# Kernel tuning notes

Measured on AMD Instinct MI355X. Metric: run time of the kernel, lower is better.

The kernel has to match this reference:

```python
import jax, jax.numpy as jnp
import numpy as np
from jax import lax

EPSILON = 1e-12


def _sobel_kernels(n1=1, n2=2, n3=2):
    Sx = np.asarray([[[-n1, 0, n1], [-n2, 0, n2], [-n1, 0, n1]],
                     [[-n2, 0, n2], [-n3 * n2, 0, n3 * n2], [-n2, 0, n2]],
                     [[-n1, 0, n1], [-n2, 0, n2], [-n1, 0, n1]]])
    Sy = np.asarray([[[-n1, -n2, -n1], [0, 0, 0], [n1, n2, n1]],
                     [[-n2, -n3 * n2, -n2], [0, 0, 0], [n2, n3 * n2, n2]],
                     [[-n1, -n2, -n1], [0, 0, 0], [n1, n2, n1]]])
    Sz = np.asarray([[[-n1, -n2, -n1], [-n2, -n3 * n2, -n2], [-n1, -n2, -n1]],
                     [[0, 0, 0], [0, 0, 0], [0, 0, 0]],
                     [[n1, n2, n1], [n2, n3 * n2, n2], [n1, n2, n1]]])
    Sd11 = np.asarray([[[0, n1, n2], [-n1, 0, n1], [-n2, -n1, 0]],
                       [[0, n2, n2 * n3], [-n2, 0, n2], [-n2 * n3, -n2, 0]],
                       [[0, n1, n2], [-n1, 0, n1], [-n2, -n1, 0]]])
    Sd12 = np.asarray([[[-n2, -n1, 0], [-n1, 0, n1], [0, n1, n2]],
                       [[-n2 * n3, -n2, 0], [-n2, 0, n2], [0, n2, n2 * n3]],
                       [[-n2, -n1, 0], [-n1, 0, n1], [0, n1, n2]]])
    Sd21 = Sd11.T
    Sd22 = Sd12.T
    Sd31 = np.asarray([-S.T for S in Sd11.T])
    Sd32 = np.asarray([S.T for S in Sd12.T])
    ks = np.stack([Sx, Sy, Sz, Sd11, Sd12, Sd21, Sd22, Sd31, Sd32]).astype(np.float32)
    return jnp.asarray(ks[:, None])  # [9, 1, 3, 3, 3] (OIDHW)


_KERNELS = _sobel_kernels(1, 2, 2)


def _edge_magnitude(img):
    # img: [B, C, H, W, D]. Per-channel convs are summed over C in the original;
    # by linearity of conv, sum channels first, then run all 9 stencils at once.
    C = img.shape[1]
    x = jnp.sum(img, axis=1, keepdims=True)  # [B, 1, H, W, D]
    g = lax.conv_general_dilated(
        x, _KERNELS, window_strides=(1, 1, 1), padding='SAME',
        dimension_numbers=('NCDHW', 'OIDHW', 'NCDHW'))  # [B, 9, H, W, D]
    mag = jnp.sqrt(jnp.sum(g * g, axis=1, keepdims=True) + EPSILON)
    return mag / C  # (1/C) * sqrt(sum_sq + eps), matches operator precedence


def setup_inputs() -> dict:
    key = jax.random.key(0)
    k1, k2 = jax.random.split(key)
    shape = (2, 2, 128, 128, 128)
    y = jax.random.normal(k1, shape, dtype=jnp.float32)
    yp = jax.random.normal(k2, shape, dtype=jnp.float32)
    return {"y": y, "yp": yp}


def reference(y, yp):
    y_edge = _edge_magnitude(y)
    yp_edge = _edge_magnitude(yp)
    return jnp.mean((y_edge - yp_edge) ** 2)  # nn.MSELoss default 'mean'
```

## Files before the change

### kernel.cpp

```cpp
#include <hip/hip_runtime.h>


namespace {

constexpr int ZDIM = 128, YDIM = 128, XDIM = 128;
constexpr int TX = 32, TY = 8, ZC = 8;
constexpr int LW = 40;
constexpr int ROWS = TY + 2;
constexpr int PLANE = ROWS * LW;
constexpr int QPR = LW / 4;
constexpr int NSLOT = ROWS * QPR;
constexpr int YX = YDIM * XDIM;
constexpr size_t CS = (size_t)ZDIM * YX;
constexpr float INV_N = 1.0f / 4194304.0f;

__device__ __forceinline__ void plane_combos(const float* __restrict__ p,
                                             float* __restrict__ C) {
  float sx[3], dx[3], ex[3];
#pragma unroll
  for (int r = 0; r < 3; ++r) {
    const float a0 = p[r * LW + 0];
    const float a1 = p[r * LW + 1];
    const float a2 = p[r * LW + 2];
    const float t = a0 + a2;
    ex[r] = t + a1;
    sx[r] = __builtin_fmaf(2.0f, a1, t);
    dx[r] = a2 - a0;
  }
  C[3] = (dx[0] + dx[2]) + dx[1];
  C[0] = C[3] + dx[1];
  C[1] = sx[2] - sx[0];
  C[5] = (sx[0] + sx[2]) + sx[1];
  C[2] = C[5] + sx[1];
  C[4] = ex[2] - ex[0];
  C[6] = __builtin_fmaf(2.0f, ex[1], ex[0] + ex[2]);
}

__device__ __forceinline__ float edge_mag_half(const float* __restrict__ Ca,
                                               const float* __restrict__ Cb,
                                               const float* __restrict__ Cc) {
  const float g1  = __builtin_fmaf(2.0f, Cb[0], Ca[0] + Cc[0]);
  const float g2  = __builtin_fmaf(2.0f, Cb[1], Ca[1] + Cc[1]);
  const float g3  = Cc[2] - Ca[2];
  const float Azx = __builtin_fmaf(2.0f, Cb[3], Ca[3] + Cc[3]);
  const float Azy = __builtin_fmaf(2.0f, Cb[4], Ca[4] + Cc[4]);
  const float Axz = Cc[5] - Ca[5];
  const float Axy = g2 - Cb[1];
  const float Ayx = g1 - Cb[0];
  const float Ayz = Cc[6] - Ca[6];
  const float g4 = Azx - Azy, g5 = Azx + Azy;
  const float g6 = Axz - Axy, g7 = Axz + Axy;
  const float g8 = Ayx - Ayz, g9 = Ayx + Ayz;
  float s = __builtin_fmaf(g1, g1, 1e-12f);
  s = __builtin_fmaf(g2, g2, s); s = __builtin_fmaf(g3, g3, s);
  s = __builtin_fmaf(g4, g4, s); s = __builtin_fmaf(g5, g5, s);
  s = __builtin_fmaf(g6, g6, s); s = __builtin_fmaf(g7, g7, s);
  s = __builtin_fmaf(g8, g8, s); s = __builtin_fmaf(g9, g9, s);
  return 0.5f * sqrtf(s);
}

__global__ __launch_bounds__(256)
void gme_loss_kernel(const float* __restrict__ y,
                     const float* __restrict__ yp,
                     float* __restrict__ out) {
  const int tx  = threadIdx.x;
  const int ty  = threadIdx.y;
  const int tid = ty * TX + tx;

  const int bx = blockIdx.x;
  const int x0 = (bx & 3) * TX;
  const int y0 = (bx >> 2) * TY;
  const int z0 = blockIdx.y * ZC;
  const int b  = blockIdx.z;

  __shared__ __align__(16) float lds[2][2][PLANE];
  __shared__ float red[4];

  const bool has_slot = tid < 2 * NSLOT;
  bool sok = false;
  const float* gp = nullptr;
  float* w0 = nullptr; float* w1 = nullptr;
  if (has_slot) {
    const int vol = tid >= NSLOT;
    const int s   = tid - vol * NSLOT;
    const int ly  = s / QPR;
    const int lx  = s - ly * QPR;
    const int py  = y0 - 1 + ly;
    const int px  = x0 - 4 + 4 * lx;
    sok = (py >= 0) & (py < YDIM) & (px >= 0) & (px <= XDIM - 4);
    const float* src = vol ? yp : y;
    gp = src + (size_t)b * 2 * CS + (size_t)py * XDIM + px;
    w0 = &lds[vol][0][ly * LW + lx * 4];
    w1 = &lds[vol][1][ly * LW + lx * 4];
  }

  const int ridx = ty * LW + tx + 3;
  const float* rY0 = &lds[0][0][ridx];
  const float* rY1 = &lds[0][1][ridx];
  const float* rP0 = &lds[1][0][ridx];
  const float* rP1 = &lds[1][1][ridx];

  auto prefetch = [&](int zc) -> float4 {
    float4 v = make_float4(0.f, 0.f, 0.f, 0.f);
    if (sok && (unsigned)zc < (unsigned)ZDIM) {
      const float* p = gp + (size_t)zc * YX;
      const float4 a = *(const float4*)p;
      const float4 c = *(const float4*)(p + CS);
      v.x = a.x + c.x; v.y = a.y + c.y; v.z = a.z + c.z; v.w = a.w + c.w;
    }
    return v;
  };

  float KY[3][7] = {}, KP[3][7] = {};
  float acc = 0.0f;

  float4 pf = prefetch(z0 - 1);

#pragma unroll
  for (int i = 0; i < ZC + 2; ++i) {
    if (has_slot) {
      float* w = (i & 1) ? w1 : w0;
      *(float4*)w = pf;
    }
    if (i < ZC + 1) pf = prefetch(z0 + i);
    __syncthreads();

    float* Cc_y = KY[i % 3];
    float* Cc_p = KP[i % 3];
    plane_combos((i & 1) ? rY1 : rY0, Cc_y);
    plane_combos((i & 1) ? rP1 : rP0, Cc_p);

    if (i >= 2) {
      const float* Ca_y = KY[(i + 1) % 3];
      const float* Cb_y = KY[(i + 2) % 3];
      const float* Ca_p = KP[(i + 1) % 3];
      const float* Cb_p = KP[(i + 2) % 3];
      const float my = edge_mag_half(Ca_y, Cb_y, Cc_y);
      const float mp = edge_mag_half(Ca_p, Cb_p, Cc_p);
      const float d = my - mp;
      acc = __builtin_fmaf(d, d, acc);
    }
  }

#pragma unroll
  for (int off = 32; off > 0; off >>= 1) acc += __shfl_down(acc, off);
  const int lane = tid & 63;
  const int wave = tid >> 6;
  if (lane == 0) red[wave] = acc;
  __syncthreads();
  if (tid == 0) {
    const float s = (red[0] + red[1] + red[2] + red[3]) * INV_N;
    atomicAdd(out, s);
  }
}

}

extern "C" void kernel_launch(void* const* d_in, const int* in_sizes, int n_in,
                              void* d_out, int out_size, void* d_ws, size_t ws_size,
                              hipStream_t stream) {
  const float* y  = (const float*)d_in[0];
  const float* yp = (const float*)d_in[1];
  float* out = (float*)d_out;

  hipMemsetAsync(out, 0, sizeof(float), stream);

  dim3 block(TX, TY, 1);
  dim3 grid((XDIM / TX) * (YDIM / TY),
            ZDIM / ZC,
            2);
  gme_loss_kernel<<<grid, block, 0, stream>>>(y, yp, out);
}
```

Baseline: 131.4 us.

## Process two z-planes per barrier with four-slot LDS ring and longer z-chunks

Doubles the z-chunk per block from 8 to 16 planes, which cuts the redundant halo loads per output plane, and halves the grid along z. Each iteration now stores two prefetched planes into a four-deep LDS ring and handles both after a single barrier, halving the number of __syncthreads calls and letting two global loads per thread be in flight at once. In exchange, LDS use doubles, live registers increase, and there are fewer blocks to spread across the GPU.

```diff
diff --git a/kernel.cpp b/kernel.cpp
--- a/kernel.cpp
+++ b/kernel.cpp
@@ -4,7 +4,7 @@
 namespace {
 
 constexpr int ZDIM = 128, YDIM = 128, XDIM = 128;
-constexpr int TX = 32, TY = 8, ZC = 8;
+constexpr int TX = 32, TY = 8, ZC = 16;
 constexpr int LW = 40;
 constexpr int ROWS = TY + 2;
 constexpr int PLANE = ROWS * LW;
@@ -13,6 +13,7 @@
 constexpr int YX = YDIM * XDIM;
 constexpr size_t CS = (size_t)ZDIM * YX;
 constexpr float INV_N = 1.0f / 4194304.0f;
+constexpr int NW = (ZC + 2) / 2;
 
 __device__ __forceinline__ void plane_combos(const float* __restrict__ p,
                                              float* __restrict__ C) {
@@ -73,13 +74,13 @@
   const int z0 = blockIdx.y * ZC;
   const int b  = blockIdx.z;
 
-  __shared__ __align__(16) float lds[2][2][PLANE];
+  __shared__ __align__(16) float lds[2][4][PLANE];
   __shared__ float red[4];
 
   const bool has_slot = tid < 2 * NSLOT;
   bool sok = false;
   const float* gp = nullptr;
-  float* w0 = nullptr; float* w1 = nullptr;
+  float* wbase = nullptr;
   if (has_slot) {
     const int vol = tid >= NSLOT;
     const int s   = tid - vol * NSLOT;
@@ -90,15 +91,10 @@
     sok = (py >= 0) & (py < YDIM) & (px >= 0) & (px <= XDIM - 4);
     const float* src = vol ? yp : y;
     gp = src + (size_t)b * 2 * CS + (size_t)py * XDIM + px;
-    w0 = &lds[vol][0][ly * LW + lx * 4];
-    w1 = &lds[vol][1][ly * LW + lx * 4];
+    wbase = &lds[vol][0][ly * LW + lx * 4];
   }
 
-  const int ridx = ty * LW + tx + 3;
-  const float* rY0 = &lds[0][0][ridx];
-  const float* rY1 = &lds[0][1][ridx];
-  const float* rP0 = &lds[1][0][ridx];
-  const float* rP1 = &lds[1][1][ridx];
+  const float* rb = &lds[0][0][ty * LW + tx + 3];
 
   auto prefetch = [&](int zc) -> float4 {
     float4 v = make_float4(0.f, 0.f, 0.f, 0.f);
@@ -114,31 +110,39 @@
   float KY[3][7] = {}, KP[3][7] = {};
   float acc = 0.0f;
 
-  float4 pf = prefetch(z0 - 1);
+  float4 pfA = prefetch(z0 - 1);
+  float4 pfB = prefetch(z0);
 
 #pragma unroll
-  for (int i = 0; i < ZC + 2; ++i) {
+  for (int i = 0; i < NW; ++i) {
+    const int j0 = 2 * i;
     if (has_slot) {
-      float* w = (i & 1) ? w1 : w0;
-      *(float4*)w = pf;
+      *(float4*)(wbase + (j0 & 3) * PLANE)       = pfA;
+      *(float4*)(wbase + ((j0 + 1) & 3) * PLANE) = pfB;
     }
-    if (i < ZC + 1) pf = prefetch(z0 + i);
+    if (i < NW - 1) {
+      pfA = prefetch(z0 + 1 + j0);
+      pfB = prefetch(z0 + 2 + j0);
+    }
     __syncthreads();
 
-    float* Cc_y = KY[i % 3];
-    float* Cc_p = KP[i % 3];
-    plane_combos((i & 1) ? rY1 : rY0, Cc_y);
-    plane_combos((i & 1) ? rP1 : rP0, Cc_p);
-
-    if (i >= 2) {
-      const float* Ca_y = KY[(i + 1) % 3];
-      const float* Cb_y = KY[(i + 2) % 3];
-      const float* Ca_p = KP[(i + 1) % 3];
-      const float* Cb_p = KP[(i + 2) % 3];
-      const float my = edge_mag_half(Ca_y, Cb_y, Cc_y);
-      const float mp = edge_mag_half(Ca_p, Cb_p, Cc_p);
-      const float d = my - mp;
-      acc = __builtin_fmaf(d, d, acc);
+#pragma unroll
+    for (int k = 0; k < 2; ++k) {
+      const int j = j0 + k;
+      float* Cc_y = KY[j % 3];
+      float* Cc_p = KP[j % 3];
+      plane_combos(rb + (j & 3) * PLANE, Cc_y);
+      plane_combos(rb + (4 + (j & 3)) * PLANE, Cc_p);
+      if (j >= 2) {
+        const float* Ca_y = KY[(j + 1) % 3];
+        const float* Cb_y = KY[(j + 2) % 3];
+        const float* Ca_p = KP[(j + 1) % 3];
+        const float* Cb_p = KP[(j + 2) % 3];
+        const float my = edge_mag_half(Ca_y, Cb_y, Cc_y);
+        const float mp = edge_mag_half(Ca_p, Cb_p, Cc_p);
+        const float d = my - mp;
+        acc = __builtin_fmaf(d, d, acc);
+      }
     }
   }
 
```

Result: faster. 120.8 us (-8.0%).

## Replace LDS plane staging with direct global row loads and cross-lane bpermute

Applied to the files above, without the earlier changes.

Drops the shared-memory plane buffers and the per-plane __syncthreads. Each wave now owns one 64-wide x row and loads the y-1, y and y+1 rows of both channels straight from global memory into registers, double-buffered one z-plane ahead. X-neighbour values come from other lanes through ds_bpermute, and the two edge lanes load the halo columns themselves. Tile shape and z depth also change, to 64x4 with 16 planes per block. This removes LDS traffic and barrier stalls, at the cost of three times the row loads (which rely on cache), scalar rather than float4 loads, more register use and predicated halo loads in the edge lanes.

```diff
diff --git a/kernel.cpp b/kernel.cpp
--- a/kernel.cpp
+++ b/kernel.cpp
@@ -4,36 +4,19 @@
 namespace {
 
 constexpr int ZDIM = 128, YDIM = 128, XDIM = 128;
-constexpr int TX = 32, TY = 8, ZC = 8;
-constexpr int LW = 40;
-constexpr int ROWS = TY + 2;
-constexpr int PLANE = ROWS * LW;
-constexpr int QPR = LW / 4;
-constexpr int NSLOT = ROWS * QPR;
+constexpr int TX = 64, TY = 4, ZC = 16;
 constexpr int YX = YDIM * XDIM;
 constexpr size_t CS = (size_t)ZDIM * YX;
 constexpr float INV_N = 1.0f / 4194304.0f;
 
-__device__ __forceinline__ void plane_combos(const float* __restrict__ p,
-                                             float* __restrict__ C) {
-  float sx[3], dx[3], ex[3];
-#pragma unroll
-  for (int r = 0; r < 3; ++r) {
-    const float a0 = p[r * LW + 0];
-    const float a1 = p[r * LW + 1];
-    const float a2 = p[r * LW + 2];
-    const float t = a0 + a2;
-    ex[r] = t + a1;
-    sx[r] = __builtin_fmaf(2.0f, a1, t);
-    dx[r] = a2 - a0;
-  }
-  C[3] = (dx[0] + dx[2]) + dx[1];
-  C[0] = C[3] + dx[1];
-  C[1] = sx[2] - sx[0];
-  C[5] = (sx[0] + sx[2]) + sx[1];
-  C[2] = C[5] + sx[1];
-  C[4] = ex[2] - ex[0];
-  C[6] = __builtin_fmaf(2.0f, ex[1], ex[0] + ex[2]);
+__device__ __forceinline__ float ldz(const float* p, bool ok) {
+  float v = 0.0f;
+  if (ok) v = *p;
+  return v;
+}
+
+__device__ __forceinline__ float bperm(int addr, float v) {
+  return __int_as_float(__builtin_amdgcn_ds_bpermute(addr, __float_as_int(v)));
 }
 
 __device__ __forceinline__ float edge_mag_half(const float* __restrict__ Ca,
@@ -63,90 +46,133 @@
 void gme_loss_kernel(const float* __restrict__ y,
                      const float* __restrict__ yp,
                      float* __restrict__ out) {
-  const int tx  = threadIdx.x;
-  const int ty  = threadIdx.y;
-  const int tid = ty * TX + tx;
+  const int lane = threadIdx.x;
+  const int ty   = threadIdx.y;
+  const int tid  = ty * TX + lane;
 
   const int bx = blockIdx.x;
-  const int x0 = (bx & 3) * TX;
-  const int y0 = (bx >> 2) * TY;
+  const int x0 = (bx & 1) * TX;
+  const int yy = (bx >> 1) * TY + ty;
   const int z0 = blockIdx.y * ZC;
   const int b  = blockIdx.z;
 
-  __shared__ __align__(16) float lds[2][2][PLANE];
-  __shared__ float red[4];
+  const float* Y0 = y  + (size_t)b * 2 * CS;
+  const float* Y1 = Y0 + CS;
+  const float* P0 = yp + (size_t)b * 2 * CS;
+  const float* P1 = P0 + CS;
 
-  const bool has_slot = tid < 2 * NSLOT;
-  bool sok = false;
-  const float* gp = nullptr;
-  float* w0 = nullptr; float* w1 = nullptr;
-  if (has_slot) {
-    const int vol = tid >= NSLOT;
-    const int s   = tid - vol * NSLOT;
-    const int ly  = s / QPR;
-    const int lx  = s - ly * QPR;
-    const int py  = y0 - 1 + ly;
-    const int px  = x0 - 4 + 4 * lx;
-    sok = (py >= 0) & (py < YDIM) & (px >= 0) & (px <= XDIM - 4);
-    const float* src = vol ? yp : y;
-    gp = src + (size_t)b * 2 * CS + (size_t)py * XDIM + px;
-    w0 = &lds[vol][0][ly * LW + lx * 4];
-    w1 = &lds[vol][1][ly * LW + lx * 4];
-  }
+  const int xg  = x0 + lane;
+  const int vox = yy * XDIM + xg;
+  const bool okM0 = (yy > 0);
+  const bool okP0 = (yy < YDIM - 1);
 
-  const int ridx = ty * LW + tx + 3;
-  const float* rY0 = &lds[0][0][ridx];
-  const float* rY1 = &lds[0][1][ridx];
-  const float* rP0 = &lds[1][0][ridx];
-  const float* rP1 = &lds[1][1][ridx];
+  const bool left  = (lane == 0);
+  const bool right = (lane == TX - 1);
+  const int  hx    = left ? (x0 - 1) : (x0 + TX);
+  const int  hvox  = yy * XDIM + hx;
+  const bool hok0  = (left && x0 > 0) || (right && x0 + TX < XDIM);
 
-  auto prefetch = [&](int zc) -> float4 {
-    float4 v = make_float4(0.f, 0.f, 0.f, 0.f);
-    if (sok && (unsigned)zc < (unsigned)ZDIM) {
-      const float* p = gp + (size_t)zc * YX;
-      const float4 a = *(const float4*)p;
-      const float4 c = *(const float4*)(p + CS);
-      v.x = a.x + c.x; v.y = a.y + c.y; v.z = a.z + c.z; v.w = a.w + c.w;
-    }
-    return v;
-  };
+  const int addrL = (lane > 0 ? lane - 1 : 0) << 2;
+  const int addrR = (lane < TX - 1 ? lane + 1 : TX - 1) << 2;
 
+  float pf[2][12];
+  float ph[2][12];
   float KY[3][7] = {}, KP[3][7] = {};
   float acc = 0.0f;
 
-  float4 pf = prefetch(z0 - 1);
+  auto loadPlane = [&](int buf, int zc) {
+    const bool zok = (unsigned)zc < (unsigned)ZDIM;
+    const int  zca = zok ? zc : 0;
+    const int  o   = zca * YX + vox;
+    const bool okC = zok, okM = zok && okM0, okP = zok && okP0;
+    pf[buf][0]  = ldz(Y0 + (o - XDIM), okM);
+    pf[buf][1]  = ldz(Y1 + (o - XDIM), okM);
+    pf[buf][2]  = ldz(Y0 + o,          okC);
+    pf[buf][3]  = ldz(Y1 + o,          okC);
+    pf[buf][4]  = ldz(Y0 + (o + XDIM), okP);
+    pf[buf][5]  = ldz(Y1 + (o + XDIM), okP);
+    pf[buf][6]  = ldz(P0 + (o - XDIM), okM);
+    pf[buf][7]  = ldz(P1 + (o - XDIM), okM);
+    pf[buf][8]  = ldz(P0 + o,          okC);
+    pf[buf][9]  = ldz(P1 + o,          okC);
+    pf[buf][10] = ldz(P0 + (o + XDIM), okP);
+    pf[buf][11] = ldz(P1 + (o + XDIM), okP);
+    const int  h  = zca * YX + hvox;
+    const bool hC = zok && hok0, hM = hC && okM0, hP = hC && okP0;
+    ph[buf][0]  = ldz(Y0 + (h - XDIM), hM);
+    ph[buf][1]  = ldz(Y1 + (h - XDIM), hM);
+    ph[buf][2]  = ldz(Y0 + h,          hC);
+    ph[buf][3]  = ldz(Y1 + h,          hC);
+    ph[buf][4]  = ldz(Y0 + (h + XDIM), hP);
+    ph[buf][5]  = ldz(Y1 + (h + XDIM), hP);
+    ph[buf][6]  = ldz(P0 + (h - XDIM), hM);
+    ph[buf][7]  = ldz(P1 + (h - XDIM), hM);
+    ph[buf][8]  = ldz(P0 + h,          hC);
+    ph[buf][9]  = ldz(P1 + h,          hC);
+    ph[buf][10] = ldz(P0 + (h + XDIM), hP);
+    ph[buf][11] = ldz(P1 + (h + XDIM), hP);
+  };
+
+  auto volCombos = [&](float m0, float m1, float c0, float c1, float q0, float q1,
+                       float hys, float hyd, float hye, float* __restrict__ C) {
+    const float vm = m0 + m1, v0 = c0 + c1, vp = q0 + q1;
+    const float t  = vm + vp;
+    const float ys = __builtin_fmaf(2.0f, v0, t);
+    const float yd = vp - vm;
+    const float ye = t + v0;
+    float ysL = bperm(addrL, ys), ysR = bperm(addrR, ys);
+    float ydL = bperm(addrL, yd), ydR = bperm(addrR, yd);
+    float yeL = bperm(addrL, ye), yeR = bperm(addrR, ye);
+    ysL = left ? hys : ysL;   ysR = right ? hys : ysR;
+    ydL = left ? hyd : ydL;   ydR = right ? hyd : ydR;
+    yeL = left ? hye : yeL;   yeR = right ? hye : yeR;
+    const float tS = ysL + ysR, tD = ydL + ydR, tE = yeL + yeR;
+    C[0] = ysR - ysL;
+    C[2] = __builtin_fmaf(2.0f, ys, tS);
+    C[6] = tS + ys;
+    C[1] = __builtin_fmaf(2.0f, yd, tD);
+    C[4] = tD + yd;
+    C[3] = yeR - yeL;
+    C[5] = __builtin_fmaf(2.0f, ye, tE);
+  };
+
+  loadPlane(0, z0 - 1);
 
 #pragma unroll
-  for (int i = 0; i < ZC + 2; ++i) {
-    if (has_slot) {
-      float* w = (i & 1) ? w1 : w0;
-      *(float4*)w = pf;
+  for (int j = 0; j < ZC + 2; ++j) {
+    const int cur = j & 1;
+    if (j < ZC + 1) loadPlane(cur ^ 1, z0 + j);
+
+    float* Cy = KY[j % 3];
+    float* Cp = KP[j % 3];
+    {
+      const float hvm = ph[cur][0] + ph[cur][1];
+      const float hv0 = ph[cur][2] + ph[cur][3];
+      const float hvp = ph[cur][4] + ph[cur][5];
+      const float ht  = hvm + hvp;
+      volCombos(pf[cur][0], pf[cur][1], pf[cur][2], pf[cur][3], pf[cur][4], pf[cur][5],
+                __builtin_fmaf(2.0f, hv0, ht), hvp - hvm, ht + hv0, Cy);
     }
-    if (i < ZC + 1) pf = prefetch(z0 + i);
-    __syncthreads();
-
-    float* Cc_y = KY[i % 3];
-    float* Cc_p = KP[i % 3];
-    plane_combos((i & 1) ? rY1 : rY0, Cc_y);
-    plane_combos((i & 1) ? rP1 : rP0, Cc_p);
-
-    if (i >= 2) {
-      const float* Ca_y = KY[(i + 1) % 3];
-      const float* Cb_y = KY[(i + 2) % 3];
-      const float* Ca_p = KP[(i + 1) % 3];
-      const float* Cb_p = KP[(i + 2) % 3];
-      const float my = edge_mag_half(Ca_y, Cb_y, Cc_y);
-      const float mp = edge_mag_half(Ca_p, Cb_p, Cc_p);
+    {
+      const float hvm = ph[cur][6] + ph[cur][7];
+      const float hv0 = ph[cur][8] + ph[cur][9];
+      const float hvp = ph[cur][10] + ph[cur][11];
+      const float ht  = hvm + hvp;
+      volCombos(pf[cur][6], pf[cur][7], pf[cur][8], pf[cur][9], pf[cur][10], pf[cur][11],
+                __builtin_fmaf(2.0f, hv0, ht), hvp - hvm, ht + hv0, Cp);
+    }
+    if (j >= 2) {
+      const float my = edge_mag_half(KY[(j + 1) % 3], KY[(j + 2) % 3], Cy);
+      const float mp = edge_mag_half(KP[(j + 1) % 3], KP[(j + 2) % 3], Cp);
       const float d = my - mp;
       acc = __builtin_fmaf(d, d, acc);
     }
   }
 
+  __shared__ float red[4];
 #pragma unroll
   for (int off = 32; off > 0; off >>= 1) acc += __shfl_down(acc, off);
-  const int lane = tid & 63;
-  const int wave = tid >> 6;
-  if (lane == 0) red[wave] = acc;
+  if (lane == 0) red[ty] = acc;
   __syncthreads();
   if (tid == 0) {
     const float s = (red[0] + red[1] + red[2] + red[3]) * INV_N;
```

Measured after the change: 186.5 us. 1.42x slower.
